# Kernel optimization log

Measured on AMD Instinct MI355X. Metric: run time of the kernel, lower is better.

Reference implementation:

```python
import jax, jax.numpy as jnp
import numpy as np

N_NODES = 50000
N_EDGES = 1600000
IN_CH = 128
HID = 64
HEADS = 2
OUT_CH2 = HID // 8  # 8
OUT_FC = 1
N_GRAPHS = 64
NEG_SLOPE = 0.2


def setup_inputs() -> dict:
    key = jax.random.key(0)
    ks = jax.random.split(key, 12)
    x = jax.random.normal(ks[0], (N_NODES, IN_CH), dtype=jnp.float32)
    edge_index = jax.random.randint(ks[1], (2, N_EDGES), 0, N_NODES, dtype=jnp.int32)
    batch = jnp.sort(jax.random.randint(ks[2], (N_NODES,), 0, N_GRAPHS, dtype=jnp.int32))
    s = lambda fan: 1.0 / np.sqrt(fan)
    W1 = jax.random.normal(ks[3], (IN_CH, HEADS * HID), dtype=jnp.float32) * s(IN_CH)
    att_src1 = jax.random.normal(ks[4], (HEADS, HID), dtype=jnp.float32) * s(HID)
    att_dst1 = jax.random.normal(ks[5], (HEADS, HID), dtype=jnp.float32) * s(HID)
    b1 = jnp.zeros((HEADS * HID,), dtype=jnp.float32)
    W2 = jax.random.normal(ks[6], (HEADS * HID, OUT_CH2), dtype=jnp.float32) * s(HEADS * HID)
    att_src2 = jax.random.normal(ks[7], (1, OUT_CH2), dtype=jnp.float32) * s(OUT_CH2)
    att_dst2 = jax.random.normal(ks[8], (1, OUT_CH2), dtype=jnp.float32) * s(OUT_CH2)
    b2 = jnp.zeros((OUT_CH2,), dtype=jnp.float32)
    fcW = jax.random.normal(ks[9], (OUT_CH2, OUT_FC), dtype=jnp.float32) * s(OUT_CH2)
    fcb = jnp.zeros((OUT_FC,), dtype=jnp.float32)
    return {"x": x, "edge_index": edge_index, "batch": batch,
            "W1": W1, "att_src1": att_src1, "att_dst1": att_dst1, "b1": b1,
            "W2": W2, "att_src2": att_src2, "att_dst2": att_dst2, "b2": b2,
            "fcW": fcW, "fcb": fcb}


def gat_conv(x, edge_index, W, att_src, att_dst, bias, heads, out_ch):
    """PyG GATConv (concat=True, add_self_loops=True, negative_slope=0.2, eval mode)."""
    n = x.shape[0]
    loop = jnp.arange(n, dtype=edge_index.dtype)
    src = jnp.concatenate([edge_index[0], loop])
    dst = jnp.concatenate([edge_index[1], loop])
    h = (x @ W).reshape(n, heads, out_ch)                 # [N,H,C]
    a_src = jnp.sum(h * att_src[None], axis=-1)           # [N,H]
    a_dst = jnp.sum(h * att_dst[None], axis=-1)           # [N,H]
    logits = jax.nn.leaky_relu(a_src[src] + a_dst[dst], NEG_SLOPE)  # [E,H]
    m = jax.ops.segment_max(logits, dst, num_segments=n)  # segment softmax over dst
    e = jnp.exp(logits - m[dst])
    denom = jax.ops.segment_sum(e, dst, num_segments=n)
    alpha = e / denom[dst]                                # [E,H]
    msg = h[src] * alpha[:, :, None]                      # [E,H,C]
    out = jax.ops.segment_sum(msg, dst, num_segments=n)   # [N,H,C]
    return out.reshape(n, heads * out_ch) + bias


def reference(x, edge_index, batch, W1, att_src1, att_dst1, b1,
              W2, att_src2, att_dst2, b2, fcW, fcb):
    h = gat_conv(x, edge_index, W1, att_src1, att_dst1, b1, HEADS, HID)
    h = jax.nn.relu(h)
    h = gat_conv(h, edge_index, W2, att_src2, att_dst2, b2, 1, OUT_CH2)
    h = jax.nn.relu(h)
    # global_mean_pool over graphs
    sums = jax.ops.segment_sum(h, batch, num_segments=N_GRAPHS)
    cnts = jax.ops.segment_sum(jnp.ones((h.shape[0],), h.dtype), batch, num_segments=N_GRAPHS)
    pooled = sums / jnp.maximum(cnts, 1.0)[:, None]       # [G, OUT_CH2]
    y = pooled @ fcW + fcb
    y = 2.0 * jax.nn.sigmoid(y) - 1.0
    return y.squeeze(-1)                                  # [G]
```

## Files before the change

kernel.cpp:

```cpp
#include <hip/hip_runtime.h>
#include <math.h>

#define MAXD 96

__device__ __forceinline__ float lrelu(float v){ return v >= 0.f ? v : 0.2f * v; }

__device__ __forceinline__ unsigned short f2bf(float f){
  unsigned u = __float_as_uint(f);
  return (unsigned short)((u + 0x7fffu + ((u >> 16) & 1u)) >> 16);
}

__global__ void scanA(const int* __restrict__ deg, int* __restrict__ excl,
                      int* __restrict__ part, int n){
  __shared__ int s[256];
  int t = threadIdx.x;
  int i = blockIdx.x * 256 + t;
  int v = (i < n) ? deg[i] : 0;
  s[t] = v;
  __syncthreads();
  for (int o = 1; o < 256; o <<= 1){
    int tv = (t >= o) ? s[t - o] : 0;
    __syncthreads();
    s[t] += tv;
    __syncthreads();
  }
  if (i < n) excl[i] = s[t] - v;
  if (t == 255) part[blockIdx.x] = s[t];
}

__global__ void scanB(int* __restrict__ part, int nb){
  __shared__ int s[256];
  int t = threadIdx.x;
  int v = (t < nb) ? part[t] : 0;
  s[t] = v;
  __syncthreads();
  for (int o = 1; o < 256; o <<= 1){
    int tv = (t >= o) ? s[t - o] : 0;
    __syncthreads();
    s[t] += tv;
    __syncthreads();
  }
  if (t < nb) part[t] = s[t] - v;
}

__global__ void scanC(int* __restrict__ off, const int* __restrict__ part, int n, int ET){
  int i = blockIdx.x * 256 + threadIdx.x;
  if (i < n) off[i] += part[blockIdx.x];
  if (i == 0) off[n] = ET;
}

__global__ void scatterK(const int* __restrict__ srcA, const int* __restrict__ dstA, int E, int ET,
                         const int* __restrict__ off, const int* __restrict__ erank,
                         int* __restrict__ csrc){
  int e = blockIdx.x * blockDim.x + threadIdx.x;
  if (e >= ET) return;
  int s, d;
  if (e < E){ s = srcA[e]; d = dstA[e]; } else { s = e - E; d = s; }
  csrc[off[d] + erank[e]] = s;
}

__global__ __launch_bounds__(256, 2) void gemm1cnt(const float* __restrict__ x, const float* __restrict__ W1,
    const float* __restrict__ attS, const float* __restrict__ attD,
    unsigned short* __restrict__ h1b, float* __restrict__ a1s, float* __restrict__ a1d, int nN,
    const int* __restrict__ dstA, int E, int ET, int* __restrict__ deg, int* __restrict__ erank){
  __shared__ float4 Ws4[128][32];
  __shared__ float4 xs4[32][32];
  int t = threadIdx.x;
  int b = blockIdx.x;
  int g1b = (int)gridDim.x;
  int CH = (ET + g1b - 1) / g1b;
  int eBeg = b * CH;
  int eEnd = eBeg + CH < ET ? eBeg + CH : ET;

  auto edgeWork = [&](){
    for (int e = eBeg + t; e < eEnd; e += 256){
      int d = (e < E) ? dstA[e] : (e - E);
      erank[e] = atomicAdd(&deg[d], 1);
    }
  };

  auto gemmWork = [&](){
    const float4* Wg = reinterpret_cast<const float4*>(W1);
    #pragma unroll
    for (int i = 0; i < 16; ++i){
      int idx = t + i * 256;
      Ws4[idx >> 5][idx & 31] = Wg[idx];
    }
    int n0 = b * 32;
    const float4* xg = reinterpret_cast<const float4*>(x);
    #pragma unroll
    for (int i = 0; i < 4; ++i){
      int idx = t + i * 256;
      int r = idx >> 5, c = idx & 31;
      int gn = n0 + r; if (gn >= nN) gn = nN - 1;
      xs4[r][c ^ (r & 7)] = xg[(size_t)gn * 32 + c];
    }
    __syncthreads();
    int cb = t & 15, nl = t >> 4;
    int cb2 = cb * 2;
    int c0 = cb * 8;
    int sw = nl & 7;
    float4 accA0 = make_float4(0.f,0.f,0.f,0.f), accA1 = accA0;
    float4 accB0 = accA0, accB1 = accA0;
    #pragma unroll 2
    for (int k4 = 0; k4 < 32; ++k4){
      float4 xv0 = xs4[nl][k4 ^ sw];
      float4 xv1 = xs4[nl + 16][k4 ^ sw];
      float xa[4] = {xv0.x, xv0.y, xv0.z, xv0.w};
      float xb[4] = {xv1.x, xv1.y, xv1.z, xv1.w};
      #pragma unroll
      for (int j = 0; j < 4; ++j){
        float4 wA = Ws4[4 * k4 + j][cb2];
        float4 wB = Ws4[4 * k4 + j][cb2 + 1];
        accA0.x = fmaf(xa[j], wA.x, accA0.x);
        accA0.y = fmaf(xa[j], wA.y, accA0.y);
        accA0.z = fmaf(xa[j], wA.z, accA0.z);
        accA0.w = fmaf(xa[j], wA.w, accA0.w);
        accA1.x = fmaf(xa[j], wB.x, accA1.x);
        accA1.y = fmaf(xa[j], wB.y, accA1.y);
        accA1.z = fmaf(xa[j], wB.z, accA1.z);
        accA1.w = fmaf(xa[j], wB.w, accA1.w);
        accB0.x = fmaf(xb[j], wA.x, accB0.x);
        accB0.y = fmaf(xb[j], wA.y, accB0.y);
        accB0.z = fmaf(xb[j], wA.z, accB0.z);
        accB0.w = fmaf(xb[j], wA.w, accB0.w);
        accB1.x = fmaf(xb[j], wB.x, accB1.x);
        accB1.y = fmaf(xb[j], wB.y, accB1.y);
        accB1.z = fmaf(xb[j], wB.z, accB1.z);
        accB1.w = fmaf(xb[j], wB.w, accB1.w);
      }
    }
    float4 as0 = *reinterpret_cast<const float4*>(attS + c0);
    float4 as1 = *reinterpret_cast<const float4*>(attS + c0 + 4);
    float4 ad0 = *reinterpret_cast<const float4*>(attD + c0);
    float4 ad1 = *reinterpret_cast<const float4*>(attD + c0 + 4);
    #pragma unroll
    for (int j = 0; j < 2; ++j){
      int n = n0 + nl + j * 16;
      if (n >= nN) continue;
      float4 h0 = j ? accB0 : accA0;
      float4 h1v = j ? accB1 : accA1;
      uint4 pk;
      pk.x = (unsigned)f2bf(h0.x)  | ((unsigned)f2bf(h0.y)  << 16);
      pk.y = (unsigned)f2bf(h0.z)  | ((unsigned)f2bf(h0.w)  << 16);
      pk.z = (unsigned)f2bf(h1v.x) | ((unsigned)f2bf(h1v.y) << 16);
      pk.w = (unsigned)f2bf(h1v.z) | ((unsigned)f2bf(h1v.w) << 16);
      *reinterpret_cast<uint4*>(h1b + (size_t)n * 128 + c0) = pk;
      float s = h0.x*as0.x + h0.y*as0.y + h0.z*as0.z + h0.w*as0.w
              + h1v.x*as1.x + h1v.y*as1.y + h1v.z*as1.z + h1v.w*as1.w;
      float d = h0.x*ad0.x + h0.y*ad0.y + h0.z*ad0.z + h0.w*ad0.w
              + h1v.x*ad1.x + h1v.y*ad1.y + h1v.z*ad1.z + h1v.w*ad1.w;
      s += __shfl_xor(s, 1); s += __shfl_xor(s, 2); s += __shfl_xor(s, 4);
      d += __shfl_xor(d, 1); d += __shfl_xor(d, 2); d += __shfl_xor(d, 4);
      if ((cb & 7) == 0){
        int head = cb >> 3;
        a1s[n * 2 + head] = s;
        a1d[n * 2 + head] = d;
      }
    }
  };

  if (b & 1){ edgeWork(); gemmWork(); }
  else      { gemmWork(); edgeWork(); }
}

__global__ __launch_bounds__(256) void agg1(const int* __restrict__ off, const int* __restrict__ csrc,
    const float* __restrict__ a1s, const float* __restrict__ a1d,
    const unsigned short* __restrict__ h1b, const float* __restrict__ b1,
    const float* __restrict__ W2, const float* __restrict__ attS2, const float* __restrict__ attD2,
    float* __restrict__ h2, float* __restrict__ a2s, float* __restrict__ a2d, int nN){
  __shared__ float al[4][MAXD][2];
  __shared__ int   sidx[4][MAXD];
  int t = threadIdx.x;
  int w = t >> 6, lane = t & 63;
  int n = blockIdx.x * 4 + w;
  if (n >= nN) return;
  int start = off[n], end = off[n + 1];
  int deg = end - start;
  int degc = deg < MAXD ? deg : MAXD;
  float ad0 = a1d[2 * n], ad1 = a1d[2 * n + 1];
  float ls0 = 0.f, ls1 = 0.f;
  for (int i = lane; i < degc; i += 64){
    int s = csrc[start + i];
    sidx[w][i] = s;
    float2 as = *reinterpret_cast<const float2*>(a1s + 2 * s);
    float e0 = __expf(lrelu(as.x + ad0));
    float e1 = __expf(lrelu(as.y + ad1));
    al[w][i][0] = e0; al[w][i][1] = e1;
    ls0 += e0; ls1 += e1;
  }
  #pragma unroll
  for (int o = 32; o > 0; o >>= 1){
    ls0 += __shfl_xor(ls0, o);
    ls1 += __shfl_xor(ls1, o);
  }
  float d0 = ls0, d1 = ls1;
  int c4 = (lane & 31) * 4;
  int h = c4 >> 6;
  int sub = lane >> 5;
  float4 acc = make_float4(0.f, 0.f, 0.f, 0.f);
  #pragma unroll 8
  for (int k = 0; k < degc; k += 2){
    int e = k + sub;
    bool ok = e < degc;
    int ee = ok ? e : degc - 1;
    int s = sidx[w][ee];
    float wgt = ok ? al[w][ee][h] : 0.f;
    uint2 v = *reinterpret_cast<const uint2*>(h1b + (size_t)s * 128 + c4);
    acc.x = fmaf(wgt, __uint_as_float(v.x << 16),         acc.x);
    acc.y = fmaf(wgt, __uint_as_float(v.x & 0xffff0000u), acc.y);
    acc.z = fmaf(wgt, __uint_as_float(v.y << 16),         acc.z);
    acc.w = fmaf(wgt, __uint_as_float(v.y & 0xffff0000u), acc.w);
  }
  acc.x += __shfl_xor(acc.x, 32);
  acc.y += __shfl_xor(acc.y, 32);
  acc.z += __shfl_xor(acc.z, 32);
  acc.w += __shfl_xor(acc.w, 32);
  float inv = 1.f / (h ? d1 : d0);
  float4 bb = *reinterpret_cast<const float4*>(b1 + c4);
  float oj[4];
  oj[0] = fmaxf(fmaf(acc.x, inv, bb.x), 0.f);
  oj[1] = fmaxf(fmaf(acc.y, inv, bb.y), 0.f);
  oj[2] = fmaxf(fmaf(acc.z, inv, bb.z), 0.f);
  oj[3] = fmaxf(fmaf(acc.w, inv, bb.w), 0.f);
  const float4* W2v = reinterpret_cast<const float4*>(W2);
  float p8[8] = {0.f,0.f,0.f,0.f,0.f,0.f,0.f,0.f};
  #pragma unroll
  for (int j = 0; j < 4; ++j){
    float4 wlo = W2v[(c4 + j) * 2];
    float4 whi = W2v[(c4 + j) * 2 + 1];
    p8[0] = fmaf(oj[j], wlo.x, p8[0]); p8[1] = fmaf(oj[j], wlo.y, p8[1]);
    p8[2] = fmaf(oj[j], wlo.z, p8[2]); p8[3] = fmaf(oj[j], wlo.w, p8[3]);
    p8[4] = fmaf(oj[j], whi.x, p8[4]); p8[5] = fmaf(oj[j], whi.y, p8[5]);
    p8[6] = fmaf(oj[j], whi.z, p8[6]); p8[7] = fmaf(oj[j], whi.w, p8[7]);
  }
  #pragma unroll
  for (int o = 16; o > 0; o >>= 1){
    #pragma unroll
    for (int cc = 0; cc < 8; ++cc) p8[cc] += __shfl_xor(p8[cc], o);
  }
  if (lane == 0){
    *reinterpret_cast<float4*>(h2 + (size_t)n * 8)     = make_float4(p8[0], p8[1], p8[2], p8[3]);
    *reinterpret_cast<float4*>(h2 + (size_t)n * 8 + 4) = make_float4(p8[4], p8[5], p8[6], p8[7]);
    float s2 = 0.f, dd2 = 0.f;
    #pragma unroll
    for (int cc = 0; cc < 8; ++cc){
      s2  = fmaf(p8[cc], attS2[cc], s2);
      dd2 = fmaf(p8[cc], attD2[cc], dd2);
    }
    a2s[n] = s2; a2d[n] = dd2;
  }
}

__global__ __launch_bounds__(256) void agg2(const int* __restrict__ off, const int* __restrict__ csrc,
    const float* __restrict__ a2s, const float* __restrict__ a2d,
    const float* __restrict__ h2, const float* __restrict__ b2, float* __restrict__ out2, int nN){
  __shared__ float al[4][MAXD];
  __shared__ int sidx[4][MAXD];
  int t = threadIdx.x;
  int w = t >> 6, lane = t & 63;
  int n = blockIdx.x * 4 + w;
  if (n >= nN) return;
  int start = off[n], end = off[n + 1];
  int deg = end - start, degc = deg < MAXD ? deg : MAXD;
  float ad = a2d[n];
  float ls = 0.f;
  for (int i = lane; i < degc; i += 64){
    int s = csrc[start + i];
    sidx[w][i] = s;
    float e = __expf(lrelu(a2s[s] + ad));
    al[w][i] = e;
    ls += e;
  }
  #pragma unroll
  for (int o = 32; o > 0; o >>= 1) ls += __shfl_xor(ls, o);
  float dv = ls;
  int c = lane & 7, eb = lane >> 3;
  float acc = 0.f;
  #pragma unroll 4
  for (int k = 0; k < degc; k += 8){
    int e = k + eb;
    bool ok = e < degc;
    int ee = ok ? e : degc - 1;
    float wgt = ok ? al[w][ee] : 0.f;
    acc = fmaf(wgt, h2[(size_t)sidx[w][ee] * 8 + c], acc);
  }
  acc += __shfl_xor(acc, 8);
  acc += __shfl_xor(acc, 16);
  acc += __shfl_xor(acc, 32);
  if (lane < 8) out2[(size_t)n * 8 + lane] = fmaxf(acc / dv + b2[lane], 0.f);
}

__global__ __launch_bounds__(256) void poolFC(const float* __restrict__ out2,
    const int* __restrict__ batch, const float* __restrict__ fcW,
    const float* __restrict__ fcb, float* __restrict__ out, int nN){
  __shared__ float red[256];
  int g = blockIdx.x;
  int lo = 0, hi = nN;
  while (lo < hi){ int m = (lo + hi) >> 1; if (batch[m] < g) lo = m + 1; else hi = m; }
  int s = lo;
  hi = nN;
  while (lo < hi){ int m = (lo + hi) >> 1; if (batch[m] < g + 1) lo = m + 1; else hi = m; }
  int e = lo;
  int t = threadIdx.x;
  int c = t & 7, row = t >> 3;
  float acc = 0.f;
  for (int i = s + row; i < e; i += 32) acc += out2[(size_t)i * 8 + c];
  red[t] = acc;
  __syncthreads();
  for (int o = 128; o >= 8; o >>= 1){
    if (t < o) red[t] += red[t + o];
    __syncthreads();
  }
  if (t == 0){
    float cc = fmaxf((float)(e - s), 1.0f);
    float y = fcb[0];
    #pragma unroll
    for (int c2 = 0; c2 < 8; ++c2) y += (red[c2] / cc) * fcW[c2];
    out[g] = 2.f / (1.f + expf(-y)) - 1.f;
  }
}

extern "C" void kernel_launch(void* const* d_in, const int* in_sizes, int n_in,
                              void* d_out, int out_size, void* d_ws, size_t ws_size,
                              hipStream_t stream){
  const float* x    = (const float*)d_in[0];
  const int*   ei   = (const int*)d_in[1];
  const int*   batch= (const int*)d_in[2];
  const float* W1   = (const float*)d_in[3];
  const float* aS1  = (const float*)d_in[4];
  const float* aD1  = (const float*)d_in[5];
  const float* b1   = (const float*)d_in[6];
  const float* W2   = (const float*)d_in[7];
  const float* aS2  = (const float*)d_in[8];
  const float* aD2  = (const float*)d_in[9];
  const float* b2   = (const float*)d_in[10];
  const float* fcW  = (const float*)d_in[11];
  const float* fcb  = (const float*)d_in[12];
  float* out = (float*)d_out;

  const int N  = in_sizes[0] / 128;
  const int E  = in_sizes[1] / 2;
  const int ET = E + N;
  const int G  = 64;

  const int* eiSrc = ei;
  const int* eiDst = ei + E;

  char* w = (char*)d_ws;
  size_t o = 0;
  auto alloc = [&](size_t bytes)->char*{
    o = (o + 255) & ~(size_t)255;
    char* p = w + o;
    o += bytes;
    return p;
  };
  int*   deg    = (int*)  alloc((size_t)N * 4);
  size_t zbytes = (size_t)N * 4;
  int*   csrOff = (int*)  alloc((size_t)(N + 1) * 4);
  int*   part   = (int*)  alloc(256 * 4);
  int*   erank  = (int*)  alloc((size_t)ET * 4);
  int*   csrc   = (int*)  alloc((size_t)ET * 4);
  unsigned short* h1b = (unsigned short*)alloc((size_t)N * 128 * 2);
  float* a1s    = (float*)alloc((size_t)N * 2 * 4);
  float* a1d    = (float*)alloc((size_t)N * 2 * 4);
  float* h2     = (float*)alloc((size_t)N * 8 * 4);
  float* a2s    = (float*)alloc((size_t)N * 4);
  float* a2d    = (float*)alloc((size_t)N * 4);
  float* out2   = (float*)alloc((size_t)N * 8 * 4);
  (void)ws_size; (void)n_in; (void)out_size;

  hipMemsetAsync(deg, 0, zbytes, stream);

  int ebl = (ET + 255) / 256;
  int nbl = (N + 255) / 256;
  int g1b = (N + 31) / 32;

  gemm1cnt<<<g1b, 256, 0, stream>>>(x, W1, aS1, aD1, h1b, a1s, a1d, N,
                                    eiDst, E, ET, deg, erank);
  scanA   <<<nbl, 256, 0, stream>>>(deg, csrOff, part, N);
  scanB   <<<1,   256, 0, stream>>>(part, nbl);
  scanC   <<<nbl, 256, 0, stream>>>(csrOff, part, N, ET);
  scatterK<<<ebl, 256, 0, stream>>>(eiSrc, eiDst, E, ET, csrOff, erank, csrc);

  agg1 <<<(N + 3) / 4, 256, 0, stream>>>(csrOff, csrc, a1s, a1d, h1b, b1, W2, aS2, aD2, h2, a2s, a2d, N);
  agg2 <<<(N + 3) / 4, 256, 0, stream>>>(csrOff, csrc, a2s, a2d, h2, b2, out2, N);
  poolFC<<<G, 256, 0, stream>>>(out2, batch, fcW, fcb, out, N);
}
```

Baseline: 237.2 us.

## Quantize layer-1 features to int8 with per-head scales and merge scan kernels

The GEMM epilogue now stores the layer-1 node features as int8, using one symmetric scale per node and head (its max-abs divided by 127), in place of bf16. The scale is packed next to the source attention logit in a float4, and the aggregation folds it into the edge weight. This halves the bytes gathered per edge in the bandwidth-bound agg1 kernel. In exchange it loses precision: int8 keeps less accuracy than bf16, and an outlier can crush the other values in its group. Separately, the scanB and scanC kernels are fused into one kernel in which every block re-scans the partial sums, which saves one launch.

```diff
diff --git a/kernel.cpp b/kernel.cpp
--- a/kernel.cpp
+++ b/kernel.cpp
@@ -4,11 +4,6 @@
 #define MAXD 96
 
 __device__ __forceinline__ float lrelu(float v){ return v >= 0.f ? v : 0.2f * v; }
-
-__device__ __forceinline__ unsigned short f2bf(float f){
-  unsigned u = __float_as_uint(f);
-  return (unsigned short)((u + 0x7fffu + ((u >> 16) & 1u)) >> 16);
-}
 
 __global__ void scanA(const int* __restrict__ deg, int* __restrict__ excl,
                       int* __restrict__ part, int n){
@@ -28,10 +23,11 @@
   if (t == 255) part[blockIdx.x] = s[t];
 }
 
-__global__ void scanB(int* __restrict__ part, int nb){
+__global__ void scanBC(int* __restrict__ csrOff, const int* __restrict__ part,
+                       int n, int ET, int nbl){
   __shared__ int s[256];
-  int t = threadIdx.x;
-  int v = (t < nb) ? part[t] : 0;
+  int t = threadIdx.x, b = blockIdx.x;
+  int v = (t < nbl) ? part[t] : 0;
   s[t] = v;
   __syncthreads();
   for (int o = 1; o < 256; o <<= 1){
@@ -40,13 +36,10 @@
     s[t] += tv;
     __syncthreads();
   }
-  if (t < nb) part[t] = s[t] - v;
-}
-
-__global__ void scanC(int* __restrict__ off, const int* __restrict__ part, int n, int ET){
-  int i = blockIdx.x * 256 + threadIdx.x;
-  if (i < n) off[i] += part[blockIdx.x];
-  if (i == 0) off[n] = ET;
+  int add = (b > 0) ? s[b - 1] : 0;
+  int i = b * 256 + t;
+  if (i < n) csrOff[i] += add;
+  if (i == 0) csrOff[n] = ET;
 }
 
 __global__ void scatterK(const int* __restrict__ srcA, const int* __restrict__ dstA, int E, int ET,
@@ -61,7 +54,7 @@
 
 __global__ __launch_bounds__(256, 2) void gemm1cnt(const float* __restrict__ x, const float* __restrict__ W1,
     const float* __restrict__ attS, const float* __restrict__ attD,
-    unsigned short* __restrict__ h1b, float* __restrict__ a1s, float* __restrict__ a1d, int nN,
+    unsigned char* __restrict__ h1q, float* __restrict__ a1sc, float* __restrict__ a1d, int nN,
     const int* __restrict__ dstA, int E, int ET, int* __restrict__ deg, int* __restrict__ erank){
   __shared__ float4 Ws4[128][32];
   __shared__ float4 xs4[32][32];
@@ -140,22 +133,33 @@
       if (n >= nN) continue;
       float4 h0 = j ? accB0 : accA0;
       float4 h1v = j ? accB1 : accA1;
-      uint4 pk;
-      pk.x = (unsigned)f2bf(h0.x)  | ((unsigned)f2bf(h0.y)  << 16);
-      pk.y = (unsigned)f2bf(h0.z)  | ((unsigned)f2bf(h0.w)  << 16);
-      pk.z = (unsigned)f2bf(h1v.x) | ((unsigned)f2bf(h1v.y) << 16);
-      pk.w = (unsigned)f2bf(h1v.z) | ((unsigned)f2bf(h1v.w) << 16);
-      *reinterpret_cast<uint4*>(h1b + (size_t)n * 128 + c0) = pk;
       float s = h0.x*as0.x + h0.y*as0.y + h0.z*as0.z + h0.w*as0.w
               + h1v.x*as1.x + h1v.y*as1.y + h1v.z*as1.z + h1v.w*as1.w;
       float d = h0.x*ad0.x + h0.y*ad0.y + h0.z*ad0.z + h0.w*ad0.w
               + h1v.x*ad1.x + h1v.y*ad1.y + h1v.z*ad1.z + h1v.w*ad1.w;
-      s += __shfl_xor(s, 1); s += __shfl_xor(s, 2); s += __shfl_xor(s, 4);
-      d += __shfl_xor(d, 1); d += __shfl_xor(d, 2); d += __shfl_xor(d, 4);
+      float am = fmaxf(fmaxf(fmaxf(fabsf(h0.x), fabsf(h0.y)), fmaxf(fabsf(h0.z), fabsf(h0.w))),
+                       fmaxf(fmaxf(fabsf(h1v.x), fabsf(h1v.y)), fmaxf(fabsf(h1v.z), fabsf(h1v.w))));
+      #pragma unroll
+      for (int o = 1; o <= 4; o <<= 1){
+        s += __shfl_xor(s, o);
+        d += __shfl_xor(d, o);
+        am = fmaxf(am, __shfl_xor(am, o));
+      }
+      float scale = am * (1.f / 127.f);
+      float qs = am > 0.f ? 127.f / am : 0.f;
+      int q0 = __float2int_rn(h0.x * qs),  q1 = __float2int_rn(h0.y * qs);
+      int q2 = __float2int_rn(h0.z * qs),  q3 = __float2int_rn(h0.w * qs);
+      int q4 = __float2int_rn(h1v.x * qs), q5 = __float2int_rn(h1v.y * qs);
+      int q6 = __float2int_rn(h1v.z * qs), q7 = __float2int_rn(h1v.w * qs);
+      uint2 pk;
+      pk.x = (q0 & 255) | ((q1 & 255) << 8) | ((q2 & 255) << 16) | ((q3 & 255) << 24);
+      pk.y = (q4 & 255) | ((q5 & 255) << 8) | ((q6 & 255) << 16) | ((q7 & 255) << 24);
+      *reinterpret_cast<uint2*>(h1q + (size_t)n * 128 + c0) = pk;
       if ((cb & 7) == 0){
         int head = cb >> 3;
-        a1s[n * 2 + head] = s;
-        a1d[n * 2 + head] = d;
+        a1sc[n * 4 + head]     = s;
+        a1sc[n * 4 + 2 + head] = scale;
+        a1d[n * 2 + head]      = d;
       }
     }
   };
@@ -165,8 +169,8 @@
 }
 
 __global__ __launch_bounds__(256) void agg1(const int* __restrict__ off, const int* __restrict__ csrc,
-    const float* __restrict__ a1s, const float* __restrict__ a1d,
-    const unsigned short* __restrict__ h1b, const float* __restrict__ b1,
+    const float* __restrict__ a1sc, const float* __restrict__ a1d,
+    const unsigned char* __restrict__ h1q, const float* __restrict__ b1,
     const float* __restrict__ W2, const float* __restrict__ attS2, const float* __restrict__ attD2,
     float* __restrict__ h2, float* __restrict__ a2s, float* __restrict__ a2d, int nN){
   __shared__ float al[4][MAXD][2];
@@ -183,10 +187,11 @@
   for (int i = lane; i < degc; i += 64){
     int s = csrc[start + i];
     sidx[w][i] = s;
-    float2 as = *reinterpret_cast<const float2*>(a1s + 2 * s);
-    float e0 = __expf(lrelu(as.x + ad0));
-    float e1 = __expf(lrelu(as.y + ad1));
-    al[w][i][0] = e0; al[w][i][1] = e1;
+    float4 v = *reinterpret_cast<const float4*>(a1sc + 4 * s);
+    float e0 = __expf(lrelu(v.x + ad0));
+    float e1 = __expf(lrelu(v.y + ad1));
+    al[w][i][0] = e0 * v.z;
+    al[w][i][1] = e1 * v.w;
     ls0 += e0; ls1 += e1;
   }
   #pragma unroll
@@ -206,11 +211,15 @@
     int ee = ok ? e : degc - 1;
     int s = sidx[w][ee];
     float wgt = ok ? al[w][ee][h] : 0.f;
-    uint2 v = *reinterpret_cast<const uint2*>(h1b + (size_t)s * 128 + c4);
-    acc.x = fmaf(wgt, __uint_as_float(v.x << 16),         acc.x);
-    acc.y = fmaf(wgt, __uint_as_float(v.x & 0xffff0000u), acc.y);
-    acc.z = fmaf(wgt, __uint_as_float(v.y << 16),         acc.z);
-    acc.w = fmaf(wgt, __uint_as_float(v.y & 0xffff0000u), acc.w);
+    unsigned v = *reinterpret_cast<const unsigned*>(h1q + (size_t)s * 128 + c4);
+    int b0 = (int)(char)(v & 255);
+    int b1i = (int)(char)((v >> 8) & 255);
+    int b2 = (int)(char)((v >> 16) & 255);
+    int b3 = (int)(char)(v >> 24);
+    acc.x = fmaf(wgt, (float)b0,  acc.x);
+    acc.y = fmaf(wgt, (float)b1i, acc.y);
+    acc.z = fmaf(wgt, (float)b2,  acc.z);
+    acc.w = fmaf(wgt, (float)b3,  acc.w);
   }
   acc.x += __shfl_xor(acc.x, 32);
   acc.y += __shfl_xor(acc.y, 32);
@@ -361,8 +370,8 @@
   int*   part   = (int*)  alloc(256 * 4);
   int*   erank  = (int*)  alloc((size_t)ET * 4);
   int*   csrc   = (int*)  alloc((size_t)ET * 4);
-  unsigned short* h1b = (unsigned short*)alloc((size_t)N * 128 * 2);
-  float* a1s    = (float*)alloc((size_t)N * 2 * 4);
+  unsigned char* h1q = (unsigned char*)alloc((size_t)N * 128);
+  float* a1sc   = (float*)alloc((size_t)N * 4 * 4);
   float* a1d    = (float*)alloc((size_t)N * 2 * 4);
   float* h2     = (float*)alloc((size_t)N * 8 * 4);
   float* a2s    = (float*)alloc((size_t)N * 4);
@@ -376,14 +385,13 @@
   int nbl = (N + 255) / 256;
   int g1b = (N + 31) / 32;
 
-  gemm1cnt<<<g1b, 256, 0, stream>>>(x, W1, aS1, aD1, h1b, a1s, a1d, N,
+  gemm1cnt<<<g1b, 256, 0, stream>>>(x, W1, aS1, aD1, h1q, a1sc, a1d, N,
                                     eiDst, E, ET, deg, erank);
   scanA   <<<nbl, 256, 0, stream>>>(deg, csrOff, part, N);
-  scanB   <<<1,   256, 0, stream>>>(part, nbl);
-  scanC   <<<nbl, 256, 0, stream>>>(csrOff, part, N, ET);
+  scanBC  <<<nbl, 256, 0, stream>>>(csrOff, part, N, ET, nbl);
   scatterK<<<ebl, 256, 0, stream>>>(eiSrc, eiDst, E, ET, csrOff, erank, csrc);
 
-  agg1 <<<(N + 3) / 4, 256, 0, stream>>>(csrOff, csrc, a1s, a1d, h1b, b1, W2, aS2, aD2, h2, a2s, a2d, N);
+  agg1 <<<(N + 3) / 4, 256, 0, stream>>>(csrOff, csrc, a1sc, a1d, h1q, b1, W2, aS2, aD2, h2, a2s, a2d, N);
   agg2 <<<(N + 3) / 4, 256, 0, stream>>>(csrOff, csrc, a2s, a2d, h2, b2, out2, N);
   poolFC<<<G, 256, 0, stream>>>(out2, batch, fcW, fcb, out, N);
 }
```

Result: faster. 222.4 us (median of 2 runs) (-6.3%).
